# Kernel optimization log

Measured on AMD Instinct MI355X. Metric: run time of the kernel, lower is better.

Reference implementation:

```python
import jax, jax.numpy as jnp
import numpy as np

N_NODES = 20000
N_EDGES = 320000
N_GRAPHS = 512
N_FEAT = 29
DIMS = [N_FEAT, 1024, 512, 256, 512, 1024]
EPS = 1e-5


def setup_inputs() -> dict:
    key = jax.random.key(0)
    ks = jax.random.split(key, 32)
    inp = {}
    inp["x"] = jax.random.normal(ks[0], (N_NODES, N_FEAT), dtype=jnp.float32)
    inp["edge_index"] = jax.random.randint(ks[1], (2, N_EDGES), 0, N_NODES, dtype=jnp.int64)
    inp["batch"] = jnp.sort(jax.random.randint(ks[2], (N_NODES,), 0, N_GRAPHS, dtype=jnp.int64))
    # 5 GCNConv layers: weight [in, out] + bias, plus BN gamma/beta
    for i in range(5):
        din, dout = DIMS[i], DIMS[i + 1]
        inp[f"W{i+1}"] = jax.random.normal(ks[3 + i], (din, dout), dtype=jnp.float32) * (1.0 / np.sqrt(din))
        inp[f"b{i+1}"] = jnp.zeros((dout,), dtype=jnp.float32)
        inp[f"g{i+1}"] = jnp.ones((dout,), dtype=jnp.float32)
        inp[f"be{i+1}"] = jnp.zeros((dout,), dtype=jnp.float32)
    # attention gate Linear(1024, 1)
    inp["Wg"] = jax.random.normal(ks[10], (1024, 1), dtype=jnp.float32) * 0.03
    inp["bg"] = jnp.zeros((1,), dtype=jnp.float32)
    # MLP head
    inp["Wf2"] = jax.random.normal(ks[11], (1024, 128), dtype=jnp.float32) * 0.03
    inp["bf2"] = jnp.zeros((128,), dtype=jnp.float32)
    inp["Wf3"] = jax.random.normal(ks[12], (128, 16), dtype=jnp.float32) * 0.25
    inp["bf3"] = jnp.zeros((16,), dtype=jnp.float32)
    inp["Wf4"] = jax.random.normal(ks[13], (16, 1), dtype=jnp.float32) * 0.25
    inp["bf4"] = jnp.zeros((1,), dtype=jnp.float32)
    return inp


def _gcn_conv(x, row, col, W, b):
    # PyG GCNConv: linear transform, then D^{-1/2}(A+I)D^{-1/2} aggregation, then bias.
    n = x.shape[0]
    xw = x @ W  # [N, dout]
    deg = jax.ops.segment_sum(jnp.ones_like(col, dtype=xw.dtype), col, num_segments=n)
    dinv = jnp.where(deg > 0, jax.lax.rsqrt(deg), 0.0)
    norm = dinv[row] * dinv[col]  # [E+N]
    out = jax.ops.segment_sum(xw[row] * norm[:, None], col, num_segments=n)
    return out + b


def _bn_train(x, gamma, beta):
    m = jnp.mean(x, axis=0)
    v = jnp.var(x, axis=0)  # biased, matches torch training normalization
    return gamma * (x - m) * jax.lax.rsqrt(v + EPS) + beta


def _global_attention(x, batch, Wg, bg, n_graphs):
    gate = (x @ Wg + bg)[:, 0]  # [N]
    gmax = jax.ops.segment_max(gate, batch, num_segments=n_graphs)
    e = jnp.exp(gate - gmax[batch])
    s = jax.ops.segment_sum(e, batch, num_segments=n_graphs)
    alpha = e / s[batch]
    return jax.ops.segment_sum(alpha[:, None] * x, batch, num_segments=n_graphs)


def reference(x, edge_index, batch,
              W1, b1, g1, be1, W2, b2, g2, be2, W3, b3, g3, be3,
              W4, b4, g4, be4, W5, b5, g5, be5,
              Wg, bg, Wf2, bf2, Wf3, bf3, Wf4, bf4):
    n = x.shape[0]
    sl = jnp.arange(n, dtype=edge_index.dtype)
    row = jnp.concatenate([edge_index[0], sl])  # with self-loops
    col = jnp.concatenate([edge_index[1], sl])
    h = x
    params = [(W1, b1, g1, be1), (W2, b2, g2, be2), (W3, b3, g3, be3),
              (W4, b4, g4, be4), (W5, b5, g5, be5)]
    for (W, b, g, be) in params:
        h = jax.nn.relu(_gcn_conv(h, row, col, W, b))
        h = _bn_train(h, g, be)
    p = _global_attention(h, batch, Wg, bg, N_GRAPHS)  # [G, 1024]
    p = jax.nn.relu(p @ Wf2 + bf2)
    p = jax.nn.relu(p @ Wf3 + bf3)
    return p @ Wf4 + bf4  # [G, 1]
```

## Files before the change

kernel.cpp:

```cpp
#include <hip/hip_runtime.h>

#define EPS_BN 1e-5f

constexpr int NN   = 20000;
constexpr int NE   = 320000;
constexpr int NTOT = NE + NN;
constexpr int NG   = 512;
constexpr int MPAD = 20480;
constexpr int NBLK = 79;

typedef _Float16 half8  __attribute__((ext_vector_type(8)));
typedef _Float16 half2v __attribute__((ext_vector_type(2)));
typedef float floatx4   __attribute__((ext_vector_type(4)));

__device__ __forceinline__ void gload_lds16(const void* g, void* l) {
  __builtin_amdgcn_global_load_lds(
      (const __attribute__((address_space(1))) void*)g,
      (__attribute__((address_space(3))) void*)l, 16, 0, 0);
}

__global__ void k_deg(const int* __restrict__ col, int* __restrict__ deg,
                      const int* __restrict__ batch, int* __restrict__ gcnt) {
  int e = blockIdx.x * blockDim.x + threadIdx.x;
  if (e >= NTOT) return;
  int c = (e < NE) ? col[e] : (e - NE);
  atomicAdd(&deg[c], 1);
  if (e < NN) atomicAdd(&gcnt[batch[e]], 1);
}

__global__ __launch_bounds__(256) void k_pre1(const int* __restrict__ deg,
                                              float* __restrict__ dinvv,
                                              int* __restrict__ psum) {
  __shared__ int ws[4];
  int t = threadIdx.x, lane = t & 63, wv = t >> 6;
  int idx = blockIdx.x * 256 + t;
  int d = (idx < NN) ? deg[idx] : 0;
  if (idx < NN) dinvv[idx] = rsqrtf((float)d);
  int s = d;
  for (int o = 1; o < 64; o <<= 1) { int u = __shfl_up(s, o, 64); if (lane >= o) s += u; }
  if (lane == 63) ws[wv] = s;
  __syncthreads();
  if (t == 0) psum[blockIdx.x] = ws[0] + ws[1] + ws[2] + ws[3];
}

__global__ __launch_bounds__(256) void k_pre2(const int* __restrict__ psum,
                                              int* __restrict__ pbase,
                                              const int* __restrict__ gcnt,
                                              int* __restrict__ goff) {
  __shared__ int ws[8];
  int t = threadIdx.x, lane = t & 63, wv = t >> 6;
  int v = (t < NBLK) ? psum[t] : 0;
  int inc = v;
  for (int o = 1; o < 64; o <<= 1) { int u = __shfl_up(inc, o, 64); if (lane >= o) inc += u; }
  if (lane == 63) ws[wv] = inc;
  __syncthreads();
  int base = 0;
  for (int w = 0; w < wv; ++w) base += ws[w];
  int excl = base + inc - v;
  if (t < NBLK) pbase[t] = excl;
  if (t == NBLK - 1) pbase[NBLK] = excl + v;
  __syncthreads();
  int a0 = gcnt[2 * t], a1 = gcnt[2 * t + 1];
  int p = a0 + a1;
  int incp = p;
  for (int o = 1; o < 64; o <<= 1) { int u = __shfl_up(incp, o, 64); if (lane >= o) incp += u; }
  if (lane == 63) ws[4 + wv] = incp;
  __syncthreads();
  int gb = 0;
  for (int w = 0; w < wv; ++w) gb += ws[4 + w];
  int exclp = gb + incp - p;
  goff[2 * t]     = exclp;
  goff[2 * t + 1] = exclp + a0;
  if (t == 255) goff[NG] = exclp + p;
}

__global__ __launch_bounds__(256) void k_pre3(const int* __restrict__ deg,
                                              const int* __restrict__ pbase,
                                              int* __restrict__ indptr,
                                              int* __restrict__ cursor) {
  __shared__ int ws[4];
  int t = threadIdx.x, lane = t & 63, wv = t >> 6;
  int idx = blockIdx.x * 256 + t;
  int d = (idx < NN) ? deg[idx] : 0;
  int inc = d;
  for (int o = 1; o < 64; o <<= 1) { int u = __shfl_up(inc, o, 64); if (lane >= o) inc += u; }
  if (lane == 63) ws[wv] = inc;
  __syncthreads();
  int base = pbase[blockIdx.x];
  for (int w = 0; w < wv; ++w) base += ws[w];
  int excl = base + inc - d;
  if (idx < NN) { indptr[idx] = excl; cursor[idx] = excl; }
  if (idx == NN - 1) indptr[NN] = excl + d;
}

__global__ void k_fill(const int* __restrict__ row, const int* __restrict__ col,
                       const float* __restrict__ dinv, int* __restrict__ cursor,
                       int2* __restrict__ csw, float* __restrict__ rsum) {
  int e = blockIdx.x * blockDim.x + threadIdx.x;
  if (e >= NTOT) return;
  int r, c;
  if (e < NE) { r = row[e]; c = col[e]; } else { r = c = e - NE; }
  float wv = dinv[r] * dinv[c];
  int pos = atomicAdd(&cursor[c], 1);
  int2 m; m.x = r; m.y = __builtin_bit_cast(int, wv);
  csw[pos] = m;
  atomicAdd(&rsum[c], wv);
}

__global__ void k_wconv3(const float* __restrict__ W0, const float* __restrict__ W3,
                         const float* __restrict__ W4,
                         _Float16* __restrict__ T0, _Float16* __restrict__ T3,
                         _Float16* __restrict__ T4) {
  int idx = blockIdx.x * blockDim.x + threadIdx.x;
  if (idx < 32768) {
    int n = idx >> 5, k = idx & 31;
    T0[idx] = (_Float16)((k < 29) ? W0[(size_t)k * 1024 + n] : 0.f);
  } else if (idx < 32768 + 131072) {
    int j = idx - 32768;
    int n = j >> 8, k = j & 255;
    T3[j] = (_Float16)W3[(size_t)k * 512 + n];
  } else if (idx < 32768 + 131072 + 524288) {
    int j = idx - 163840;
    int n = j >> 9, k = j & 511;
    T4[j] = (_Float16)W4[(size_t)k * 1024 + n];
  }
}

__global__ __launch_bounds__(256) void k_wfold(const float* __restrict__ W, int K, int N,
                                               const float* __restrict__ sums,
                                               const float* __restrict__ gamma,
                                               const float* __restrict__ beta,
                                               _Float16* __restrict__ T,
                                               float* __restrict__ c) {
  __shared__ float red[256];
  int n = blockIdx.x, tid = threadIdx.x;
  const float inv_n = 1.f / NN;
  float csum = 0.f;
  for (int k = tid; k < K; k += 256) {
    float mean = sums[k] * inv_n;
    float var  = sums[K + k] * inv_n - mean * mean;
    float sc   = gamma[k] * rsqrtf(var + EPS_BN);
    float sh   = beta[k] - mean * sc;
    float wv   = W[(size_t)k * N + n];
    T[(size_t)n * K + k] = (_Float16)(sc * wv);
    csum += sh * wv;
  }
  red[tid] = csum;
  __syncthreads();
  for (int o = 128; o > 0; o >>= 1) {
    if (tid < o) red[tid] += red[tid + o];
    __syncthreads();
  }
  if (tid == 0) c[n] = red[0];
}

#define AGG_T  128
#define AGG_CH 128
__global__ __launch_bounds__(AGG_T) void k_agg29(
    const float* __restrict__ X,
    const int* __restrict__ indptr, const int2* __restrict__ csw,
    _Float16* __restrict__ Y) {
  __shared__ int   s_src[AGG_CH];
  __shared__ float s_w[AGG_CH];
  int node = blockIdx.x;
  int tid  = threadIdx.x;
  int beg = indptr[node], end = indptr[node + 1];
  float acc = 0.f;
  for (int e0 = beg; e0 < end; e0 += AGG_CH) {
    int c = min(AGG_CH, end - e0);
    if (tid < c) {
      int2 m = csw[e0 + tid];
      s_src[tid] = m.x;
      s_w[tid]   = __builtin_bit_cast(float, m.y);
    }
    __syncthreads();
    for (int j = 0; j < c; ++j) {
      if (tid < 29) acc += s_w[j] * X[(size_t)s_src[j] * 29 + tid];
    }
    __syncthreads();
  }
  if (tid < 32) Y[(size_t)node * 32 + tid] = (tid < 29) ? (_Float16)acc : (_Float16)0.f;
}

template<int VEC, int MODE>
__global__ __launch_bounds__(256) void k_aggv(
    const _Float16* __restrict__ X, _Float16* __restrict__ Y,
    const int* __restrict__ indptr, const int2* __restrict__ csw,
    const float* __restrict__ rowsum,
    const float* __restrict__ p0, const float* __restrict__ p1,
    const float* __restrict__ p2)
{
  constexpr int F = 64 * VEC;
  int wave = threadIdx.x >> 6;
  int lane = threadIdx.x & 63;
  int node = blockIdx.x * 4 + wave;
  int beg = indptr[node], end = indptr[node + 1];
  float acc[VEC];
  #pragma unroll
  for (int i = 0; i < VEC; ++i) acc[i] = 0.f;
  const unsigned* Xl = (const unsigned*)X + lane * (VEC / 2);

  auto body = [&](int e) {
    int2 m = csw[e];
    float we = __builtin_bit_cast(float, m.y);
    const unsigned* xr = Xl + (size_t)m.x * (F / 2);
    unsigned uu[VEC / 2];
    if constexpr (VEC == 8) {
      uint4 d = *(const uint4*)xr;
      uu[0] = d.x; uu[1] = d.y; uu[2] = d.z; uu[3] = d.w;
    } else {
      uint2 d = *(const uint2*)xr;
      uu[0] = d.x; uu[1] = d.y;
    }
    #pragma unroll
    for (int i = 0; i < VEC / 2; ++i) {
      half2v h = __builtin_bit_cast(half2v, uu[i]);
      acc[2 * i]     = fmaf(we, (float)h[0], acc[2 * i]);
      acc[2 * i + 1] = fmaf(we, (float)h[1], acc[2 * i + 1]);
    }
  };
  int e = beg;
  for (; e + 8 <= end; e += 8) {
    body(e); body(e + 1); body(e + 2); body(e + 3);
    body(e + 4); body(e + 5); body(e + 6); body(e + 7);
  }
  for (; e < end; ++e) body(e);

  float s_n = rowsum[node];
  size_t ob = (size_t)node * F + lane * VEC;
  _Float16 outv[VEC];
  #pragma unroll
  for (int i = 0; i < VEC; ++i) {
    int f = lane * VEC + i;
    float v;
    if constexpr (MODE == 0) {
      v = fmaxf(acc[i] + s_n * p0[f] + p1[f], 0.f);
    } else {
      const float inv_n = 1.f / NN;
      float mean = p0[f] * inv_n;
      float var  = p0[F + f] * inv_n - mean * mean;
      float sc   = p1[f] * rsqrtf(var + EPS_BN);
      float sh   = p2[f] - mean * sc;
      v = sc * acc[i] + s_n * sh;
    }
    outv[i] = (_Float16)v;
  }
  if constexpr (VEC == 8) *(uint4*)(Y + ob) = *(const uint4*)outv;
  else                    *(uint2*)(Y + ob) = *(const uint2*)outv;
}

template<int BK>
__global__ __launch_bounds__(256) void k_gemm16(
    const _Float16* __restrict__ A, const _Float16* __restrict__ B,
    const float* __restrict__ bias,
    _Float16* __restrict__ Ch,
    float* __restrict__ stats,
    int N, int K, int do_relu, int nbx)
{
  __shared__ __align__(16) union UU {
    struct { _Float16 a[128 * BK]; _Float16 b[128 * BK]; } ab;
    _Float16 c[128 * 136];
  } u;
  __shared__ float sred[256];

  const int tid  = threadIdx.x;
  const int wave = tid >> 6;
  const int lane = tid & 63;

  int lin = blockIdx.x;
  int xcd = lin & 7, seq = lin >> 3;
  int bx = seq % nbx, grp = seq / nbx;
  int by = xcd + 8 * grp;
  const int row0 = by * 128;
  const int col0 = bx * 128;

  const int q  = lane >> 4;
  const int mm = lane & 15;
  const int wm = wave >> 1;
  const int wn = wave & 1;

  sred[tid] = 0.f;

  constexpr int NREP = (BK == 32) ? 2 : 4;
  constexpr int RPW  = (BK == 32) ? 16 : 8;
  const _Float16* pA[NREP];
  const _Float16* pB[NREP];
  _Float16* dstA[NREP];
  _Float16* dstB[NREP];
  {
    int rl = (BK == 32) ? (lane >> 2) : (lane >> 3);
    int cp = (BK == 32) ? (lane & 3) : (lane & 7);
    #pragma unroll
    for (int rep = 0; rep < NREP; ++rep) {
      int trow = wave * 32 + rep * RPW;
      int s = (BK == 32) ? ((lane >> 3) & 3) : ((rep & 1) * 4 + (rl >> 1));
      int csrc = cp ^ s;
      pA[rep] = A + (size_t)(row0 + trow + rl) * K + csrc * 8;
      pB[rep] = B + (size_t)(col0 + trow + rl) * K + csrc * 8;
      dstA[rep] = u.ab.a + trow * BK;
      dstB[rep] = u.ab.b + trow * BK;
    }
  }

  const int sR = (BK == 32) ? ((mm >> 1) & 3) : (mm >> 1);
  int rdA[4], rdB[4];
  #pragma unroll
  for (int i = 0; i < 4; ++i) {
    rdA[i] = (wm * 64 + i * 16 + mm) * BK;
    rdB[i] = (wn * 64 + i * 16 + mm) * BK;
  }

  floatx4 acc[4][4];
  #pragma unroll
  for (int i = 0; i < 4; ++i)
    #pragma unroll
    for (int j = 0; j < 4; ++j) acc[i][j] = floatx4{0.f, 0.f, 0.f, 0.f};

  for (int k0 = 0; k0 < K; k0 += BK) {
    #pragma unroll
    for (int rep = 0; rep < NREP; ++rep) {
      gload_lds16(pA[rep], dstA[rep]);
      gload_lds16(pB[rep], dstB[rep]);
      pA[rep] += BK; pB[rep] += BK;
    }
    __syncthreads();

    #pragma unroll
    for (int kk = 0; kk < BK / 32; ++kk) {
      int pos = ((q + 4 * kk) ^ sR) * 8;
      half8 av[4];
      #pragma unroll
      for (int i = 0; i < 4; ++i) av[i] = *(const half8*)&u.ab.a[rdA[i] + pos];
      #pragma unroll
      for (int j = 0; j < 4; ++j) {
        half8 bv = *(const half8*)&u.ab.b[rdB[j] + pos];
        #pragma unroll
        for (int i = 0; i < 4; ++i)
          acc[i][j] = __builtin_amdgcn_mfma_f32_16x16x32_f16(av[i], bv, acc[i][j], 0, 0, 0);
      }
    }
    __syncthreads();
  }

  float sloc[4]  = {0.f, 0.f, 0.f, 0.f};
  float s2loc[4] = {0.f, 0.f, 0.f, 0.f};
  #pragma unroll
  for (int j = 0; j < 4; ++j) {
    int cl = wn * 64 + j * 16 + mm;
    float bv = bias ? bias[col0 + cl] : 0.f;
    #pragma unroll
    for (int i = 0; i < 4; ++i) {
      #pragma unroll
      for (int r = 0; r < 4; ++r) {
        int rl = wm * 64 + i * 16 + q * 4 + r;
        float v = acc[i][j][r] + bv;
        if (do_relu) v = fmaxf(v, 0.f);
        u.c[rl * 136 + cl] = (_Float16)v;
        if (row0 + rl < NN) { sloc[j] += v; s2loc[j] += v * v; }
      }
    }
  }

  if (stats) {
    #pragma unroll
    for (int j = 0; j < 4; ++j) {
      float a = sloc[j], b2 = s2loc[j];
      a  += __shfl_xor(a, 16, 64);  a  += __shfl_xor(a, 32, 64);
      b2 += __shfl_xor(b2, 16, 64); b2 += __shfl_xor(b2, 32, 64);
      if (q == 0) {
        int cl = wn * 64 + j * 16 + mm;
        atomicAdd(&sred[cl], a);
        atomicAdd(&sred[128 + cl], b2);
      }
    }
  }
  __syncthreads();

  #pragma unroll
  for (int pass = 0; pass < 8; ++pass) {
    int cidx = tid + pass * 256;
    int r = cidx >> 4, kc = cidx & 15;
    int rr = row0 + r;
    if (rr < NN) {
      uint4 d = *(const uint4*)&u.c[r * 136 + kc * 8];
      *(uint4*)&Ch[(size_t)rr * N + col0 + kc * 8] = d;
    }
  }

  if (stats && tid < 128) {
    atomicAdd(&stats[col0 + tid], sred[tid]);
    atomicAdd(&stats[N + col0 + tid], sred[128 + tid]);
  }
}

__global__ __launch_bounds__(256) void k_stats16(const _Float16* __restrict__ X, int F,
                                                 float* __restrict__ sums) {
  int tid = threadIdx.x;
  int npf = F >> 8;
  float s[2] = {0.f, 0.f}, s2[2] = {0.f, 0.f};
  for (int r = blockIdx.x; r < NN; r += gridDim.x) {
    #pragma unroll
    for (int i = 0; i < 2; ++i) {
      if (i < npf) {
        float v = (float)X[(size_t)r * F + tid + i * 256];
        s[i] += v; s2[i] += v * v;
      }
    }
  }
  #pragma unroll
  for (int i = 0; i < 2; ++i) {
    if (i < npf) {
      atomicAdd(&sums[tid + i * 256], s[i]);
      atomicAdd(&sums[F + tid + i * 256], s2[i]);
    }
  }
}

__global__ __launch_bounds__(1024) void k_prep(const float* __restrict__ sums,
                                               const float* __restrict__ g5,
                                               const float* __restrict__ be5,
                                               const float* __restrict__ Wg,
                                               const float* __restrict__ bg,
                                               float* __restrict__ sc, float* __restrict__ sh,
                                               float* __restrict__ scWg, float* __restrict__ gconst) {
  __shared__ float red[1024];
  int f = threadIdx.x;
  const float inv_n = 1.f / NN;
  float mean = sums[f] * inv_n;
  float var  = sums[1024 + f] * inv_n - mean * mean;
  float s = g5[f] * rsqrtf(var + EPS_BN);
  float h = be5[f] - mean * s;
  sc[f] = s; sh[f] = h;
  float wgf = Wg[f];
  scWg[f] = s * wgf;
  red[f] = h * wgf;
  __syncthreads();
  for (int o = 512; o > 0; o >>= 1) {
    if (f < o) red[f] += red[f + o];
    __syncthreads();
  }
  if (f == 0) gconst[0] = red[0] + bg[0];
}

__global__ __launch_bounds__(256) void k_gate_aff(const _Float16* __restrict__ X,
                                                  const float* __restrict__ scWg,
                                                  const float* __restrict__ gconst,
                                                  float* __restrict__ gate) {
  __shared__ float red[256];
  int n = blockIdx.x, tid = threadIdx.x;
  int f = tid * 4;
  uint2 u = *(const uint2*)(X + (size_t)n * 1024 + f);
  half2v h0 = __builtin_bit_cast(half2v, u.x);
  half2v h1 = __builtin_bit_cast(half2v, u.y);
  float s = (float)h0[0] * scWg[f] + (float)h0[1] * scWg[f + 1]
          + (float)h1[0] * scWg[f + 2] + (float)h1[1] * scWg[f + 3];
  red[tid] = s;
  __syncthreads();
  for (int o = 128; o > 0; o >>= 1) {
    if (tid < o) red[tid] += red[tid + o];
    __syncthreads();
  }
  if (tid == 0) gate[n] = red[0] + gconst[0];
}

__global__ __launch_bounds__(64) void k_segred(const float* __restrict__ gate,
                                               const int* __restrict__ goff,
                                               float* __restrict__ gmax,
                                               float* __restrict__ gsum) {
  int g = blockIdx.x, tid = threadIdx.x;
  int beg = goff[g], end = goff[g + 1];
  float m = -3.4e38f;
  for (int n = beg + tid; n < end; n += 64) m = fmaxf(m, gate[n]);
  for (int o = 32; o > 0; o >>= 1) m = fmaxf(m, __shfl_down(m, o, 64));
  m = __shfl(m, 0, 64);
  float s = 0.f;
  for (int n = beg + tid; n < end; n += 64) s += expf(gate[n] - m);
  for (int o = 32; o > 0; o >>= 1) s += __shfl_down(s, o, 64);
  if (tid == 0) { gmax[g] = m; gsum[g] = s; }
}

__global__ __launch_bounds__(256) void k_pool_aff(const _Float16* __restrict__ X,
                                                  const float* __restrict__ gate,
                                                  const int* __restrict__ goff,
                                                  const float* __restrict__ gmax,
                                                  const float* __restrict__ gsum,
                                                  const float* __restrict__ sc,
                                                  const float* __restrict__ sh,
                                                  float* __restrict__ pooled) {
  int g = blockIdx.x, tid = threadIdx.x;
  int beg = goff[g], end = goff[g + 1];
  int f = tid * 4;
  float acc[4] = {0.f, 0.f, 0.f, 0.f};
  bool nonempty = end > beg;
  if (nonempty) {
    float m = gmax[g], inv = 1.f / gsum[g];
    for (int n = beg; n < end; ++n) {
      float a = expf(gate[n] - m) * inv;
      uint2 u = *(const uint2*)(X + (size_t)n * 1024 + f);
      half2v h0 = __builtin_bit_cast(half2v, u.x);
      half2v h1 = __builtin_bit_cast(half2v, u.y);
      acc[0] += a * (float)h0[0];
      acc[1] += a * (float)h0[1];
      acc[2] += a * (float)h1[0];
      acc[3] += a * (float)h1[1];
    }
  }
  #pragma unroll
  for (int i = 0; i < 4; ++i) {
    int ff = f + i;
    float v = nonempty ? (acc[i] * sc[ff] + sh[ff]) : 0.f;
    pooled[(size_t)g * 1024 + ff] = v;
  }
}

__global__ __launch_bounds__(128) void k_head(const float* __restrict__ pooled,
                                              const float* __restrict__ Wf2, const float* __restrict__ bf2,
                                              const float* __restrict__ Wf3, const float* __restrict__ bf3,
                                              const float* __restrict__ Wf4, const float* __restrict__ bf4,
                                              float* __restrict__ out) {
  __shared__ float sp[1024];
  __shared__ float sp2[128];
  __shared__ float sp3[16];
  int g = blockIdx.x, tid = threadIdx.x;
  #pragma unroll
  for (int i = 0; i < 8; ++i) sp[tid + i * 128] = pooled[(size_t)g * 1024 + tid + i * 128];
  __syncthreads();
  float s = bf2[tid];
  for (int k = 0; k < 1024; ++k) s += sp[k] * Wf2[k * 128 + tid];
  sp2[tid] = fmaxf(s, 0.f);
  __syncthreads();
  if (tid < 16) {
    float t = bf3[tid];
    for (int k = 0; k < 128; ++k) t += sp2[k] * Wf3[k * 16 + tid];
    sp3[tid] = fmaxf(t, 0.f);
  }
  __syncthreads();
  if (tid == 0) {
    float t = bf4[0];
    for (int k = 0; k < 16; ++k) t += sp3[k] * Wf4[k];
    out[g] = t;
  }
}

extern "C" void kernel_launch(void* const* d_in, const int* in_sizes, int n_in,
                              void* d_out, int out_size, void* d_ws, size_t ws_size,
                              hipStream_t stream) {
  const float* x     = (const float*)d_in[0];
  const int*   ei    = (const int*)d_in[1];
  const int*   batch = (const int*)d_in[2];
  const float* W[5]; const float* b[5]; const float* g[5]; const float* be[5];
  for (int l = 0; l < 5; ++l) {
    W[l]  = (const float*)d_in[3 + 4 * l];
    b[l]  = (const float*)d_in[4 + 4 * l];
    g[l]  = (const float*)d_in[5 + 4 * l];
    be[l] = (const float*)d_in[6 + 4 * l];
  }
  const float* Wg  = (const float*)d_in[23];
  const float* bg  = (const float*)d_in[24];
  const float* Wf2 = (const float*)d_in[25];
  const float* bf2 = (const float*)d_in[26];
  const float* Wf3 = (const float*)d_in[27];
  const float* bf3 = (const float*)d_in[28];
  const float* Wf4 = (const float*)d_in[29];
  const float* bf4 = (const float*)d_in[30];
  float* out = (float*)d_out;

  const int* row = ei;
  const int* col = ei + NE;

  char* base = (char*)d_ws;
  size_t off = 0;
  auto alloc = [&](size_t bytes) -> char* {
    char* p = base + off;
    off = (off + bytes + 255) & ~(size_t)255;
    return p;
  };
  _Float16*  AH  = (_Float16*)alloc((size_t)MPAD * 1024 * 2);
  _Float16*  ASM = (_Float16*)alloc((size_t)MPAD * 32 * 2);
  _Float16*  BF  = (_Float16*)alloc((size_t)NN * 512 * 2);
  _Float16*  BF2 = (_Float16*)alloc((size_t)NN * 512 * 2);
  _Float16*  H5  = (_Float16*)alloc((size_t)NN * 1024 * 2);
  const int wtsz[5] = {1024 * 32, 512 * 1024, 256 * 512, 512 * 256, 1024 * 512};
  _Float16* WT[5];
  for (int l = 0; l < 5; ++l) WT[l] = (_Float16*)alloc((size_t)wtsz[l] * 2);
  float* c2  = (float*)alloc(512 * 4);
  float* c3  = (float*)alloc(256 * 4);
  float* dinv    = (float*)alloc(NN * 4);
  int*   indptr  = (int*)alloc((NN + 1) * 4);
  int*   cursor  = (int*)alloc(NN * 4);
  int2*  csw     = (int2*)alloc((size_t)NTOT * 8);
  int*   psum    = (int*)alloc((NBLK + 1) * 4);
  int*   pbase   = (int*)alloc((NBLK + 1) * 4);
  int*   goff    = (int*)alloc((NG + 1) * 4);
  float* gate    = (float*)alloc(NN * 4);
  float* gmax    = (float*)alloc(NG * 4);
  float* gsum    = (float*)alloc(NG * 4);
  float* pooled  = (float*)alloc((size_t)NG * 1024 * 4);
  float* scv5 = (float*)alloc(1024 * 4);
  float* shv5 = (float*)alloc(1024 * 4);
  float* scWg = (float*)alloc(1024 * 4);
  float* gconst = (float*)alloc(4);
  size_t znf = 6656 + NN + NG + NN;
  float* zbase = (float*)alloc(znf * 4);
  float* bns  = zbase;
  int*   deg  = (int*)(zbase + 6656);
  int*   gcnt = (int*)(zbase + 6656 + NN);
  float* rsum = zbase + 6656 + NN + NG;
  float* bns1 = bns;
  float* bns2 = bns + 2048;
  float* bns3 = bns + 3072;
  float* bns4 = bns + 3584;
  float* bns5 = bns + 4608;

  hipMemsetAsync(zbase, 0, znf * 4, stream);
  k_deg<<<(NTOT + 255) / 256, 256, 0, stream>>>(col, deg, batch, gcnt);
  k_pre1<<<NBLK, 256, 0, stream>>>(deg, dinv, psum);
  k_pre2<<<1, 256, 0, stream>>>(psum, pbase, gcnt, goff);
  k_pre3<<<NBLK, 256, 0, stream>>>(deg, pbase, indptr, cursor);
  k_fill<<<(NTOT + 255) / 256, 256, 0, stream>>>(row, col, dinv, cursor, csw, rsum);
  k_wconv3<<<2688, 256, 0, stream>>>(W[0], W[3], W[4], WT[0], WT[3], WT[4]);

  auto gemm = [&](const _Float16* Aop, int wl, const float* bias,
                  _Float16* Ch, float* stats, int Nn, int Kk, int relu) {
    int nbx = Nn / 128;
    if (Kk == 32)
      k_gemm16<32><<<nbx * 160, 256, 0, stream>>>(Aop, WT[wl], bias, Ch, stats, Nn, Kk, relu, nbx);
    else
      k_gemm16<64><<<nbx * 160, 256, 0, stream>>>(Aop, WT[wl], bias, Ch, stats, Nn, Kk, relu, nbx);
  };

  k_agg29<<<NN, AGG_T, 0, stream>>>(x, indptr, csw, ASM);
  gemm(ASM, 0, b[0], AH, bns1, 1024, 32, 1);

  k_wfold<<<512, 256, 0, stream>>>(W[1], 1024, 512, bns1, g[0], be[0], WT[1], c2);
  gemm(AH, 1, nullptr, BF, nullptr, 512, 1024, 0);
  k_aggv<8, 0><<<NN / 4, 256, 0, stream>>>(BF, AH, indptr, csw, rsum, c2, b[1], nullptr);
  k_stats16<<<512, 256, 0, stream>>>(AH, 512, bns2);

  k_wfold<<<256, 256, 0, stream>>>(W[2], 512, 256, bns2, g[1], be[1], WT[2], c3);
  gemm(AH, 2, nullptr, BF2, nullptr, 256, 512, 0);
  k_aggv<4, 0><<<NN / 4, 256, 0, stream>>>(BF2, BF, indptr, csw, rsum, c3, b[2], nullptr);
  k_stats16<<<512, 256, 0, stream>>>(BF, 256, bns3);

  k_aggv<4, 1><<<NN / 4, 256, 0, stream>>>(BF, AH, indptr, csw, rsum, bns3, g[2], be[2]);
  gemm(AH, 3, b[3], BF2, bns4, 512, 256, 1);

  k_aggv<8, 1><<<NN / 4, 256, 0, stream>>>(BF2, AH, indptr, csw, rsum, bns4, g[3], be[3]);
  gemm(AH, 4, b[4], H5, bns5, 1024, 512, 1);

  k_prep<<<1, 1024, 0, stream>>>(bns5, g[4], be[4], Wg, bg, scv5, shv5, scWg, gconst);
  k_gate_aff<<<NN, 256, 0, stream>>>(H5, scWg, gconst, gate);
  k_segred<<<NG, 64, 0, stream>>>(gate, goff, gmax, gsum);
  k_pool_aff<<<NG, 256, 0, stream>>>(H5, gate, goff, gmax, gsum, scv5, shv5, pooled);

  k_head<<<NG, 128, 0, stream>>>(pooled, Wf2, bf2, Wf3, bf3, Wf4, bf4, out);
}
```

Before: 646.5 us.

## Parallelize 29-feature aggregation, pack two nodes per wave for 256-wide layers, fold BN prep

The first-layer aggregation now splits each node's edge list across four groups of 29 threads and reduces the partial sums in shared memory, so more of the block does work. The 256-feature aggregations use a new kernel that handles two nodes per wave with 16-byte loads, padding the shorter edge list with zero-weight iterations. The single-block BN/gate prep kernel is removed, and its scale/shift math is recomputed inline in the gate and pooling kernels. This saves a launch and a serialized tiny kernel, at the cost of redundant per-node recomputation and some divergence from unequal degree pairs.

```diff
diff --git a/kernel.cpp b/kernel.cpp
--- a/kernel.cpp
+++ b/kernel.cpp
@@ -154,16 +154,19 @@
   if (tid == 0) c[n] = red[0];
 }
 
-#define AGG_T  128
 #define AGG_CH 128
-__global__ __launch_bounds__(AGG_T) void k_agg29(
+__global__ __launch_bounds__(128) void k_agg29(
     const float* __restrict__ X,
     const int* __restrict__ indptr, const int2* __restrict__ csw,
     _Float16* __restrict__ Y) {
   __shared__ int   s_src[AGG_CH];
   __shared__ float s_w[AGG_CH];
+  __shared__ float red[128];
   int node = blockIdx.x;
   int tid  = threadIdx.x;
+  int sub  = tid / 29;
+  int feat = tid - sub * 29;
+  bool act = tid < 116;
   int beg = indptr[node], end = indptr[node + 1];
   float acc = 0.f;
   for (int e0 = beg; e0 < end; e0 += AGG_CH) {
@@ -174,15 +177,24 @@
       s_w[tid]   = __builtin_bit_cast(float, m.y);
     }
     __syncthreads();
-    for (int j = 0; j < c; ++j) {
-      if (tid < 29) acc += s_w[j] * X[(size_t)s_src[j] * 29 + tid];
+    if (act) {
+      for (int j = 0; j < c; j += 4) {
+        int jj = j + sub;
+        if (jj < c) acc += s_w[jj] * X[(size_t)s_src[jj] * 29 + feat];
+      }
     }
     __syncthreads();
   }
-  if (tid < 32) Y[(size_t)node * 32 + tid] = (tid < 29) ? (_Float16)acc : (_Float16)0.f;
-}
-
-template<int VEC, int MODE>
+  red[tid] = acc;
+  __syncthreads();
+  if (tid < 32) {
+    float v = 0.f;
+    if (tid < 29) v = red[tid] + red[29 + tid] + red[58 + tid] + red[87 + tid];
+    Y[(size_t)node * 32 + tid] = (_Float16)v;
+  }
+}
+
+template<int MODE>
 __global__ __launch_bounds__(256) void k_aggv(
     const _Float16* __restrict__ X, _Float16* __restrict__ Y,
     const int* __restrict__ indptr, const int2* __restrict__ csw,
@@ -190,30 +202,23 @@
     const float* __restrict__ p0, const float* __restrict__ p1,
     const float* __restrict__ p2)
 {
-  constexpr int F = 64 * VEC;
+  constexpr int F = 512;
   int wave = threadIdx.x >> 6;
   int lane = threadIdx.x & 63;
   int node = blockIdx.x * 4 + wave;
   int beg = indptr[node], end = indptr[node + 1];
-  float acc[VEC];
-  #pragma unroll
-  for (int i = 0; i < VEC; ++i) acc[i] = 0.f;
-  const unsigned* Xl = (const unsigned*)X + lane * (VEC / 2);
+  float acc[8];
+  #pragma unroll
+  for (int i = 0; i < 8; ++i) acc[i] = 0.f;
+  const unsigned* Xl = (const unsigned*)X + lane * 4;
 
   auto body = [&](int e) {
     int2 m = csw[e];
     float we = __builtin_bit_cast(float, m.y);
-    const unsigned* xr = Xl + (size_t)m.x * (F / 2);
-    unsigned uu[VEC / 2];
-    if constexpr (VEC == 8) {
-      uint4 d = *(const uint4*)xr;
-      uu[0] = d.x; uu[1] = d.y; uu[2] = d.z; uu[3] = d.w;
-    } else {
-      uint2 d = *(const uint2*)xr;
-      uu[0] = d.x; uu[1] = d.y;
-    }
-    #pragma unroll
-    for (int i = 0; i < VEC / 2; ++i) {
+    uint4 d = *(const uint4*)(Xl + (size_t)m.x * (F / 2));
+    unsigned uu[4] = {d.x, d.y, d.z, d.w};
+    #pragma unroll
+    for (int i = 0; i < 4; ++i) {
       half2v h = __builtin_bit_cast(half2v, uu[i]);
       acc[2 * i]     = fmaf(we, (float)h[0], acc[2 * i]);
       acc[2 * i + 1] = fmaf(we, (float)h[1], acc[2 * i + 1]);
@@ -227,11 +232,11 @@
   for (; e < end; ++e) body(e);
 
   float s_n = rowsum[node];
-  size_t ob = (size_t)node * F + lane * VEC;
-  _Float16 outv[VEC];
-  #pragma unroll
-  for (int i = 0; i < VEC; ++i) {
-    int f = lane * VEC + i;
+  size_t ob = (size_t)node * F + lane * 8;
+  _Float16 outv[8];
+  #pragma unroll
+  for (int i = 0; i < 8; ++i) {
+    int f = lane * 8 + i;
     float v;
     if constexpr (MODE == 0) {
       v = fmaxf(acc[i] + s_n * p0[f] + p1[f], 0.f);
@@ -245,8 +250,71 @@
     }
     outv[i] = (_Float16)v;
   }
-  if constexpr (VEC == 8) *(uint4*)(Y + ob) = *(const uint4*)outv;
-  else                    *(uint2*)(Y + ob) = *(const uint2*)outv;
+  *(uint4*)(Y + ob) = *(const uint4*)outv;
+}
+
+template<int MODE>
+__global__ __launch_bounds__(256) void k_aggp(
+    const _Float16* __restrict__ X, _Float16* __restrict__ Y,
+    const int* __restrict__ indptr, const int2* __restrict__ csw,
+    const float* __restrict__ rowsum,
+    const float* __restrict__ p0, const float* __restrict__ p1,
+    const float* __restrict__ p2)
+{
+  constexpr int F = 256;
+  int wave = threadIdx.x >> 6;
+  int lane = threadIdx.x & 63;
+  int half = lane >> 5;
+  int l32  = lane & 31;
+  int node = blockIdx.x * 8 + wave * 2 + half;
+  int beg = indptr[node], end = indptr[node + 1];
+  int len = end - beg;
+  int len0 = __shfl(len, 0, 64);
+  int len1 = __shfl(len, 32, 64);
+  int maxlen = max(len0, len1);
+
+  float acc[8];
+  #pragma unroll
+  for (int i = 0; i < 8; ++i) acc[i] = 0.f;
+  const unsigned* Xl = (const unsigned*)X + l32 * 4;
+
+  auto body = [&](int t) {
+    int e = beg + min(t, len - 1);
+    int2 m = csw[e];
+    float we = (t < len) ? __builtin_bit_cast(float, m.y) : 0.f;
+    uint4 d = *(const uint4*)(Xl + (size_t)m.x * (F / 2));
+    unsigned uu[4] = {d.x, d.y, d.z, d.w};
+    #pragma unroll
+    for (int i = 0; i < 4; ++i) {
+      half2v h = __builtin_bit_cast(half2v, uu[i]);
+      acc[2 * i]     = fmaf(we, (float)h[0], acc[2 * i]);
+      acc[2 * i + 1] = fmaf(we, (float)h[1], acc[2 * i + 1]);
+    }
+  };
+  int t = 0;
+  for (; t + 4 <= maxlen; t += 4) { body(t); body(t + 1); body(t + 2); body(t + 3); }
+  for (; t < maxlen; ++t) body(t);
+
+  float s_n = rowsum[node];
+  size_t ob = (size_t)node * F + l32 * 8;
+  _Float16 outv[8];
+  #pragma unroll
+  for (int i = 0; i < 8; ++i) {
+    int f = l32 * 8 + i;
+    float v;
+    if constexpr (MODE == 0) {
+      v = fmaxf(acc[i] + s_n * p0[f] + p1[f], 0.f);
+    } else {
+      const float inv_n = 1.f / NN;
+      float mean = p0[f] * inv_n;
+      float var  = p0[F + f] * inv_n - mean * mean;
+      float sc   = p1[f] * rsqrtf(var + EPS_BN);
+      float sh   = p2[f] - mean * sc;
+      v = sc * acc[i] + s_n * sh;
+    }
+    outv[i] = (_Float16)v;
+  }
+  *(uint4*)(Y + ob) = *(const uint4*)outv;
 }
 
 template<int BK>
@@ -416,51 +484,41 @@
   }
 }
 
-__global__ __launch_bounds__(1024) void k_prep(const float* __restrict__ sums,
+__global__ __launch_bounds__(256) void k_gate2(const _Float16* __restrict__ X,
+                                               const float* __restrict__ sums,
                                                const float* __restrict__ g5,
                                                const float* __restrict__ be5,
                                                const float* __restrict__ Wg,
                                                const float* __restrict__ bg,
-                                               float* __restrict__ sc, float* __restrict__ sh,
-                                               float* __restrict__ scWg, float* __restrict__ gconst) {
-  __shared__ float red[1024];
-  int f = threadIdx.x;
-  const float inv_n = 1.f / NN;
-  float mean = sums[f] * inv_n;
-  float var  = sums[1024 + f] * inv_n - mean * mean;
-  float s = g5[f] * rsqrtf(var + EPS_BN);
-  float h = be5[f] - mean * s;
-  sc[f] = s; sh[f] = h;
-  float wgf = Wg[f];
-  scWg[f] = s * wgf;
-  red[f] = h * wgf;
-  __syncthreads();
-  for (int o = 512; o > 0; o >>= 1) {
-    if (f < o) red[f] += red[f + o];
-    __syncthreads();
-  }
-  if (f == 0) gconst[0] = red[0] + bg[0];
-}
-
-__global__ __launch_bounds__(256) void k_gate_aff(const _Float16* __restrict__ X,
-                                                  const float* __restrict__ scWg,
-                                                  const float* __restrict__ gconst,
-                                                  float* __restrict__ gate) {
-  __shared__ float red[256];
+                                               float* __restrict__ gate) {
+  __shared__ float red[512];
   int n = blockIdx.x, tid = threadIdx.x;
   int f = tid * 4;
+  const float inv_n = 1.f / NN;
   uint2 u = *(const uint2*)(X + (size_t)n * 1024 + f);
   half2v h0 = __builtin_bit_cast(half2v, u.x);
   half2v h1 = __builtin_bit_cast(half2v, u.y);
-  float s = (float)h0[0] * scWg[f] + (float)h0[1] * scWg[f + 1]
-          + (float)h1[0] * scWg[f + 2] + (float)h1[1] * scWg[f + 3];
+  float xv[4] = {(float)h0[0], (float)h0[1], (float)h1[0], (float)h1[1]};
+  float s = 0.f, t = 0.f;
+  #pragma unroll
+  for (int i = 0; i < 4; ++i) {
+    int ff = f + i;
+    float mean = sums[ff] * inv_n;
+    float var  = sums[1024 + ff] * inv_n - mean * mean;
+    float sc   = g5[ff] * rsqrtf(var + EPS_BN);
+    float sh   = be5[ff] - mean * sc;
+    float wg   = Wg[ff];
+    s += xv[i] * (sc * wg);
+    t += sh * wg;
+  }
   red[tid] = s;
+  red[256 + tid] = t;
   __syncthreads();
   for (int o = 128; o > 0; o >>= 1) {
-    if (tid < o) red[tid] += red[tid + o];
+    if (tid < o) { red[tid] += red[tid + o]; red[256 + tid] += red[256 + tid + o]; }
     __syncthreads();
   }
-  if (tid == 0) gate[n] = red[0] + gconst[0];
+  if (tid == 0) gate[n] = red[0] + red[256] + bg[0];
 }
 
 __global__ __launch_bounds__(64) void k_segred(const float* __restrict__ gate,
@@ -479,17 +537,19 @@
   if (tid == 0) { gmax[g] = m; gsum[g] = s; }
 }
 
-__global__ __launch_bounds__(256) void k_pool_aff(const _Float16* __restrict__ X,
-                                                  const float* __restrict__ gate,
-                                                  const int* __restrict__ goff,
-                                                  const float* __restrict__ gmax,
-                                                  const float* __restrict__ gsum,
-                                                  const float* __restrict__ sc,
-                                                  const float* __restrict__ sh,
-                                                  float* __restrict__ pooled) {
+__global__ __launch_bounds__(256) void k_pool2(const _Float16* __restrict__ X,
+                                               const float* __restrict__ gate,
+                                               const int* __restrict__ goff,
+                                               const float* __restrict__ gmax,
+                                               const float* __restrict__ gsum,
+                                               const float* __restrict__ sums,
+                                               const float* __restrict__ g5,
+                                               const float* __restrict__ be5,
+                                               float* __restrict__ pooled) {
   int g = blockIdx.x, tid = threadIdx.x;
   int beg = goff[g], end = goff[g + 1];
   int f = tid * 4;
+  const float inv_n = 1.f / NN;
   float acc[4] = {0.f, 0.f, 0.f, 0.f};
   bool nonempty = end > beg;
   if (nonempty) {
@@ -508,7 +568,11 @@
   #pragma unroll
   for (int i = 0; i < 4; ++i) {
     int ff = f + i;
-    float v = nonempty ? (acc[i] * sc[ff] + sh[ff]) : 0.f;
+    float mean = sums[ff] * inv_n;
+    float var  = sums[1024 + ff] * inv_n - mean * mean;
+    float sc   = g5[ff] * rsqrtf(var + EPS_BN);
+    float sh   = be5[ff] - mean * sc;
+    float v = nonempty ? (acc[i] * sc + sh) : 0.f;
     pooled[(size_t)g * 1024 + ff] = v;
   }
 }
@@ -596,10 +660,6 @@
   float* gmax    = (float*)alloc(NG * 4);
   float* gsum    = (float*)alloc(NG * 4);
   float* pooled  = (float*)alloc((size_t)NG * 1024 * 4);
-  float* scv5 = (float*)alloc(1024 * 4);
-  float* shv5 = (float*)alloc(1024 * 4);
-  float* scWg = (float*)alloc(1024 * 4);
-  float* gconst = (float*)alloc(4);
   size_t znf = 6656 + NN + NG + NN;
   float* zbase = (float*)alloc(znf * 4);
   float* bns  = zbase;
@@ -629,29 +689,28 @@
       k_gemm16<64><<<nbx * 160, 256, 0, stream>>>(Aop, WT[wl], bias, Ch, stats, Nn, Kk, relu, nbx);
   };
 
-  k_agg29<<<NN, AGG_T, 0, stream>>>(x, indptr, csw, ASM);
+  k_agg29<<<NN, 128, 0, stream>>>(x, indptr, csw, ASM);
   gemm(ASM, 0, b[0], AH, bns1, 1024, 32, 1);
 
   k_wfold<<<512, 256, 0, stream>>>(W[1], 1024, 512, bns1, g[0], be[0], WT[1], c2);
   gemm(AH, 1, nullptr, BF, nullptr, 512, 1024, 0);
-  k_aggv<8, 0><<<NN / 4, 256, 0, stream>>>(BF, AH, indptr, csw, rsum, c2, b[1], nullptr);
+  k_aggv<0><<<NN / 4, 256, 0, stream>>>(BF, AH, indptr, csw, rsum, c2, b[1], nullptr);
   k_stats16<<<512, 256, 0, stream>>>(AH, 512, bns2);
 
   k_wfold<<<256, 256, 0, stream>>>(W[2], 512, 256, bns2, g[1], be[1], WT[2], c3);
   gemm(AH, 2, nullptr, BF2, nullptr, 256, 512, 0);
-  k_aggv<4, 0><<<NN / 4, 256, 0, stream>>>(BF2, BF, indptr, csw, rsum, c3, b[2], nullptr);
+  k_aggp<0><<<NN / 8, 256, 0, stream>>>(BF2, BF, indptr, csw, rsum, c3, b[2], nullptr);
   k_stats16<<<512, 256, 0, stream>>>(BF, 256, bns3);
 
-  k_aggv<4, 1><<<NN / 4, 256, 0, stream>>>(BF, AH, indptr, csw, rsum, bns3, g[2], be[2]);
+  k_aggp<1><<<NN / 8, 256, 0, stream>>>(BF, AH, indptr, csw, rsum, bns3, g[2], be[2]);
   gemm(AH, 3, b[3], BF2, bns4, 512, 256, 1);
 
-  k_aggv<8, 1><<<NN / 4, 256, 0, stream>>>(BF2, AH, indptr, csw, rsum, bns4, g[3], be[3]);
+  k_aggv<1><<<NN / 4, 256, 0, stream>>>(BF2, AH, indptr, csw, rsum, bns4, g[3], be[3]);
   gemm(AH, 4, b[4], H5, bns5, 1024, 512, 1);
 
-  k_prep<<<1, 1024, 0, stream>>>(bns5, g[4], be[4], Wg, bg, scv5, shv5, scWg, gconst);
-  k_gate_aff<<<NN, 256, 0, stream>>>(H5, scWg, gconst, gate);
+  k_gate2<<<NN, 256, 0, stream>>>(H5, bns5, g[4], be[4], Wg, bg, gate);
   k_segred<<<NG, 64, 0, stream>>>(gate, goff, gmax, gsum);
-  k_pool_aff<<<NG, 256, 0, stream>>>(H5, gate, goff, gmax, gsum, scv5, shv5, pooled);
+  k_pool2<<<NG, 256, 0, stream>>>(H5, gate, goff, gmax, gsum, bns5, g[4], be[4], pooled);
 
   k_head<<<NG, 128, 0, stream>>>(pooled, Wf2, bf2, Wf3, bf3, Wf4, bf4, out);
 }
```

Result: faster. 618.1 us (-4.4%).
